# Performance work log

Hardware: AMD Instinct MI355X
Metric: run time of the kernel (lower is better)

Reference implementation:

```python
import jax, jax.numpy as jnp
import numpy as np
import math

# Dims chosen per input_specs
B, Q, S, T = 8, 64, 64, 64          # batch, queries, stat (segment) count, tokens per segment
H, DH = 8, 64                        # heads, head dim
NH = H * DH                          # num_hiddens = 512
STAT_K, TOKEN_K = 8, 16
NEG = -1e6


def setup_inputs() -> dict:
    key = jax.random.key(0)
    ks = jax.random.split(key, 11)
    f = lambda k, sh: jax.random.normal(k, sh, dtype=jnp.float32)
    w = lambda k: f(k, (NH, NH)) * 0.05  # Linear weights stored as [in, out]
    return {
        "queries": f(ks[0], (B, Q, NH)),
        "stat_keys": f(ks[1], (B, S, NH)),
        "token_keys": f(ks[2], (B * S, T, NH)),
        "values": f(ks[3], (B * S, T, NH)),
        "stat_valid_lens": jax.random.randint(ks[4], (B,), 1, S + 1, dtype=jnp.int32),
        "Wq_stat": w(ks[5]),
        "Wq_token": w(ks[6]),
        "Wk_stat": w(ks[7]),
        "Wk_token": w(ks[8]),
        "Wv": w(ks[9]),
        "Wo": w(ks[10]),
    }


def reference(queries, stat_keys, token_keys, values, stat_valid_lens,
              Wq_stat, Wq_token, Wk_stat, Wk_token, Wv, Wo):
    scale = 1.0 / math.sqrt(DH)

    def split_heads(x):  # [b, L, H*DH] -> [b, H, L, DH]
        b, L, _ = x.shape
        return x.reshape(b, L, H, DH).transpose(0, 2, 1, 3)

    q_stat = split_heads(queries @ Wq_stat)        # [B,H,Q,DH]
    q_tok = split_heads(queries @ Wq_token)        # [B,H,Q,DH]
    k_stat = split_heads(stat_keys @ Wk_stat)      # [B,H,S,DH]
    # token_keys/values come in as [B*S, T, size]; per-head layout [B,H,S,T,DH]
    k_tok = (token_keys @ Wk_token).reshape(B, S, T, H, DH).transpose(0, 3, 1, 2, 4)
    v = (values @ Wv).reshape(B, S, T, H, DH).transpose(0, 3, 1, 2, 4)

    # --- stat-level scores, valid-length mask, top-k sparsification, softmax ---
    stat_scores = jnp.einsum('bhqd,bhsd->bhqs', q_stat, k_stat) * scale  # [B,H,Q,S]
    valid = jnp.arange(S)[None, None, None, :] < stat_valid_lens[:, None, None, None]
    stat_scores = jnp.where(valid, stat_scores, NEG)
    k1 = min(S - 1, STAT_K)
    _, top_idx = jax.lax.top_k(stat_scores, k1)                           # [B,H,Q,k1]
    keep = jax.nn.one_hot(top_idx, S, dtype=stat_scores.dtype).sum(-2) > 0  # [B,H,Q,S]
    stat_w = jax.nn.softmax(jnp.where(keep, stat_scores, NEG), axis=-1)   # [B,H,Q,S]

    # --- token-level scores. NOTE: the original code computes torch.topk but then
    # overwrites with the LAST k2 positions (token_weights[:, :, -k2:] = ...), so the
    # token top-k result is dead code; we faithfully reproduce the last-k2 masking. ---
    tok_scores = jnp.einsum('bhqd,bhstd->bhsqt', q_tok, k_tok) * scale    # [B,H,S,Q,T]
    k2 = min(T - 1, TOKEN_K)
    last_mask = jnp.arange(T) >= (T - k2)
    tok_w = jax.nn.softmax(jnp.where(last_mask, tok_scores, NEG), axis=-1)
    tok_w = tok_w.transpose(0, 1, 3, 2, 4)                                # [B,H,Q,S,T]

    # --- combine hierarchy and attend over values ---
    comb = stat_w[..., None] * tok_w                                      # [B,H,Q,S,T]
    out = jnp.einsum('bhqst,bhstd->bhqd', comb, v)                        # [B,H,Q,DH]
    out = out.transpose(0, 2, 1, 3).reshape(B, Q, NH)
    return out @ Wo
```

## Files before the change

kernel.cpp:

```cpp
#include <hip/hip_runtime.h>
#include <hip/hip_bf16.h>

#define BB 8
#define QQ 64
#define SS 64
#define TT 64
#define HH 8
#define DH 64
#define NHID 512
#define STAT_K 8
#define TOKEN_K 16

typedef short bf16x8 __attribute__((ext_vector_type(8)));
typedef float f32x4 __attribute__((ext_vector_type(4)));

__device__ inline ushort f2bf_rne(float x) {
    union { float f; unsigned u; } v; v.f = x;
    unsigned r = v.u + 0x7fff + ((v.u >> 16) & 1);
    return (ushort)(r >> 16);
}
__device__ inline float bf2f(ushort h) {
    union { unsigned u; float f; } v; v.u = ((unsigned)h) << 16;
    return v.f;
}

__global__ __launch_bounds__(256) void conv_all(
    const float* w0, const float* w1, const float* w2,
    const float* w3, const float* w4, const float* w5,
    const float* queries, const float* stat_keys,
    ushort* wT, ushort* q_hi, ushort* q_lo, ushort* sk_hi, ushort* sk_lo)
{
    const int z = blockIdx.z;
    if (z < 6) {
        const float* srcs[6] = {w0, w1, w2, w3, w4, w5};
        const float* src = srcs[z];
        ushort* hi = wT + (size_t)z * 524288;
        ushort* lo = hi + 262144;
        __shared__ float t[32][33];
        const int c0 = blockIdx.x * 32, r0 = blockIdx.y * 32;
        const int tx = threadIdx.x & 31, ty = threadIdx.x >> 5;
        #pragma unroll
        for (int i = 0; i < 4; ++i)
            t[ty + 8 * i][tx] = src[(r0 + ty + 8 * i) * 512 + c0 + tx];
        __syncthreads();
        #pragma unroll
        for (int i = 0; i < 4; ++i) {
            float x = t[tx][ty + 8 * i];
            ushort h = f2bf_rne(x);
            int o = (c0 + ty + 8 * i) * 512 + r0 + tx;
            hi[o] = h;
            lo[o] = f2bf_rne(x - bf2f(h));
        }
    } else {
        const float* src = (z == 6) ? queries : stat_keys;
        ushort* hi = (z == 6) ? q_hi : sk_hi;
        ushort* lo = (z == 6) ? q_lo : sk_lo;
        int base = (blockIdx.y * 16 + blockIdx.x) * 1024 + threadIdx.x * 4;
        float4 x = *(const float4*)(src + base);
        ushort4 h, l;
        h.x = f2bf_rne(x.x); l.x = f2bf_rne(x.x - bf2f(h.x));
        h.y = f2bf_rne(x.y); l.y = f2bf_rne(x.y - bf2f(h.y));
        h.z = f2bf_rne(x.z); l.z = f2bf_rne(x.z - bf2f(h.z));
        h.w = f2bf_rne(x.w); l.w = f2bf_rne(x.w - bf2f(h.w));
        *(ushort4*)(hi + base) = h;
        *(ushort4*)(lo + base) = l;
    }
}

__global__ __launch_bounds__(256) void gemm_split3(
    const ushort* __restrict__ q_hi, const ushort* __restrict__ q_lo,
    const ushort* __restrict__ sk_hi, const ushort* __restrict__ sk_lo,
    const ushort* __restrict__ wT,
    float* __restrict__ q_stat, float* __restrict__ k_stat,
    float* __restrict__ q_tokf)
{
    const int z = blockIdx.z;
    const ushort* Ah = (z == 1) ? sk_hi : q_hi;
    const ushort* Al = (z == 1) ? sk_lo : q_lo;
    const ushort* Bh = wT + (size_t)z * 524288;
    const ushort* Bl = Bh + 262144;
    float* C = (z == 0) ? q_stat : (z == 1) ? k_stat : q_tokf;
    const int K = 512, N = 512;

    __shared__ ushort As[2][64][40];
    __shared__ ushort Bs[2][64][40];
    const int tid = threadIdx.x;
    const int row0 = blockIdx.y * 64, col0 = blockIdx.x * 64;
    const int wave = tid >> 6, lane = tid & 63;
    const int wm = wave & 1, wn = wave >> 1;
    const int m16 = lane & 15, quad = lane >> 4;
    const int srow = tid >> 2, schunk = tid & 3;

    f32x4 acc[2][2];
    #pragma unroll
    for (int i = 0; i < 2; ++i)
        #pragma unroll
        for (int j = 0; j < 2; ++j)
            #pragma unroll
            for (int r = 0; r < 4; ++r) acc[i][j][r] = 0.f;

    for (int k0 = 0; k0 < K; k0 += 32) {
        const size_t aoff = (size_t)(row0 + srow) * K + k0 + schunk * 8;
        const size_t boff = (size_t)(col0 + srow) * K + k0 + schunk * 8;
        *(uint4*)&As[0][srow][schunk * 8] = *(const uint4*)(Ah + aoff);
        *(uint4*)&Bs[0][srow][schunk * 8] = *(const uint4*)(Bh + boff);
        *(uint4*)&As[1][srow][schunk * 8] = *(const uint4*)(Al + aoff);
        *(uint4*)&Bs[1][srow][schunk * 8] = *(const uint4*)(Bl + boff);
        __syncthreads();

        bf16x8 af[2], bf[2], afl[2], bfl[2];
        #pragma unroll
        for (int i = 0; i < 2; ++i) {
            af[i]  = *(const bf16x8*)&As[0][wm * 32 + i * 16 + m16][quad * 8];
            bf[i]  = *(const bf16x8*)&Bs[0][wn * 32 + i * 16 + m16][quad * 8];
            afl[i] = *(const bf16x8*)&As[1][wm * 32 + i * 16 + m16][quad * 8];
            bfl[i] = *(const bf16x8*)&Bs[1][wn * 32 + i * 16 + m16][quad * 8];
        }
        #pragma unroll
        for (int i = 0; i < 2; ++i)
            #pragma unroll
            for (int j = 0; j < 2; ++j) {
                acc[i][j] = __builtin_amdgcn_mfma_f32_16x16x32_bf16(af[i], bf[j], acc[i][j], 0, 0, 0);
                acc[i][j] = __builtin_amdgcn_mfma_f32_16x16x32_bf16(af[i], bfl[j], acc[i][j], 0, 0, 0);
                acc[i][j] = __builtin_amdgcn_mfma_f32_16x16x32_bf16(afl[i], bf[j], acc[i][j], 0, 0, 0);
            }
        __syncthreads();
    }

    #pragma unroll
    for (int i = 0; i < 2; ++i)
        #pragma unroll
        for (int j = 0; j < 2; ++j) {
            int r0 = row0 + wm * 32 + i * 16 + quad * 4;
            int c = col0 + wn * 32 + j * 16 + m16;
            #pragma unroll
            for (int reg = 0; reg < 4; ++reg)
                C[(size_t)(r0 + reg) * N + c] = acc[i][j][reg];
        }
}

__global__ __launch_bounds__(256) void gemm_out(
    const ushort* __restrict__ Ah, const ushort* __restrict__ Al,
    const ushort* __restrict__ Bh, const ushort* __restrict__ Bl,
    float* __restrict__ C)
{
    const int K = 512, N = 512;
    __shared__ ushort As[2][64][40];
    __shared__ ushort Bs[2][64][40];
    const int tid = threadIdx.x;
    const int row0 = blockIdx.y * 64, col0 = blockIdx.x * 64;
    const int wave = tid >> 6, lane = tid & 63;
    const int wm = wave & 1, wn = wave >> 1;
    const int m16 = lane & 15, quad = lane >> 4;
    const int srow = tid >> 2, schunk = tid & 3;

    f32x4 acc[2][2];
    #pragma unroll
    for (int i = 0; i < 2; ++i)
        #pragma unroll
        for (int j = 0; j < 2; ++j)
            #pragma unroll
            for (int r = 0; r < 4; ++r) acc[i][j][r] = 0.f;

    for (int k0 = 0; k0 < K; k0 += 32) {
        const size_t aoff = (size_t)(row0 + srow) * K + k0 + schunk * 8;
        const size_t boff = (size_t)(col0 + srow) * K + k0 + schunk * 8;
        *(uint4*)&As[0][srow][schunk * 8] = *(const uint4*)(Ah + aoff);
        *(uint4*)&Bs[0][srow][schunk * 8] = *(const uint4*)(Bh + boff);
        *(uint4*)&As[1][srow][schunk * 8] = *(const uint4*)(Al + aoff);
        *(uint4*)&Bs[1][srow][schunk * 8] = *(const uint4*)(Bl + boff);
        __syncthreads();

        bf16x8 af[2], bf[2], afl[2], bfl[2];
        #pragma unroll
        for (int i = 0; i < 2; ++i) {
            af[i]  = *(const bf16x8*)&As[0][wm * 32 + i * 16 + m16][quad * 8];
            bf[i]  = *(const bf16x8*)&Bs[0][wn * 32 + i * 16 + m16][quad * 8];
            afl[i] = *(const bf16x8*)&As[1][wm * 32 + i * 16 + m16][quad * 8];
            bfl[i] = *(const bf16x8*)&Bs[1][wn * 32 + i * 16 + m16][quad * 8];
        }
        #pragma unroll
        for (int i = 0; i < 2; ++i)
            #pragma unroll
            for (int j = 0; j < 2; ++j) {
                acc[i][j] = __builtin_amdgcn_mfma_f32_16x16x32_bf16(af[i], bf[j], acc[i][j], 0, 0, 0);
                acc[i][j] = __builtin_amdgcn_mfma_f32_16x16x32_bf16(af[i], bfl[j], acc[i][j], 0, 0, 0);
                acc[i][j] = __builtin_amdgcn_mfma_f32_16x16x32_bf16(afl[i], bf[j], acc[i][j], 0, 0, 0);
            }
        __syncthreads();
    }

    #pragma unroll
    for (int i = 0; i < 2; ++i)
        #pragma unroll
        for (int j = 0; j < 2; ++j) {
            int r0 = row0 + wm * 32 + i * 16 + quad * 4;
            int c = col0 + wn * 32 + j * 16 + m16;
            #pragma unroll
            for (int reg = 0; reg < 4; ++reg)
                C[(size_t)(r0 + reg) * N + c] = acc[i][j][reg];
        }
}

__global__ __launch_bounds__(256) void gemm_tok(
    const float* __restrict__ token_keys, const float* __restrict__ values,
    const ushort* __restrict__ wkt_h, const ushort* __restrict__ wv_h,
    ushort* __restrict__ k_tok, ushort* __restrict__ v_projT)
{
    const int z = blockIdx.z;
    const float* A = z ? values : token_keys;
    const ushort* Bh = z ? wv_h : wkt_h;
    const int K = 512, N = 512;

    __shared__ ushort As[64][40];
    __shared__ ushort Bs[256][40];
    const int tid = threadIdx.x;
    const int row0 = blockIdx.y * 64, col0 = blockIdx.x * 256;
    const int wave = tid >> 6, lane = tid & 63;
    const int m16 = lane & 15, quad = lane >> 4;
    const int srow = tid >> 2, schunk = tid & 3;

    const int r = row0 + srow;
    const size_t arow = (size_t)((r >> 4) * 64 + 48 + (r & 15)) * K;

    f32x4 acc[4][4];
    #pragma unroll
    for (int i = 0; i < 4; ++i)
        #pragma unroll
        for (int j = 0; j < 4; ++j)
            #pragma unroll
            for (int rr = 0; rr < 4; ++rr) acc[i][j][rr] = 0.f;

    for (int k0 = 0; k0 < K; k0 += 32) {
        const float* ap = A + arow + k0 + schunk * 8;
        float4 x0 = ((const float4*)ap)[0];
        float4 x1 = ((const float4*)ap)[1];
        ushort4 h0, h1;
        h0.x = f2bf_rne(x0.x); h0.y = f2bf_rne(x0.y);
        h0.z = f2bf_rne(x0.z); h0.w = f2bf_rne(x0.w);
        h1.x = f2bf_rne(x1.x); h1.y = f2bf_rne(x1.y);
        h1.z = f2bf_rne(x1.z); h1.w = f2bf_rne(x1.w);
        *(ushort4*)&As[srow][schunk * 8] = h0;
        *(ushort4*)&As[srow][schunk * 8 + 4] = h1;
        #pragma unroll
        for (int i = 0; i < 4; ++i) {
            int v = tid + i * 256;
            int brow = v >> 2, bchunk = v & 3;
            *(uint4*)&Bs[brow][bchunk * 8] =
                *(const uint4*)(Bh + (size_t)(col0 + brow) * K + k0 + bchunk * 8);
        }
        __syncthreads();

        bf16x8 af[4], bf[4];
        #pragma unroll
        for (int i = 0; i < 4; ++i) {
            af[i] = *(const bf16x8*)&As[i * 16 + m16][quad * 8];
            bf[i] = *(const bf16x8*)&Bs[wave * 64 + i * 16 + m16][quad * 8];
        }
        #pragma unroll
        for (int i = 0; i < 4; ++i)
            #pragma unroll
            for (int j = 0; j < 4; ++j)
                acc[i][j] = __builtin_amdgcn_mfma_f32_16x16x32_bf16(af[i], bf[j], acc[i][j], 0, 0, 0);
        __syncthreads();
    }

    #pragma unroll
    for (int i = 0; i < 4; ++i)
        #pragma unroll
        for (int j = 0; j < 4; ++j) {
            int rg = row0 + i * 16 + quad * 4;
            int c = col0 + wave * 64 + j * 16 + m16;
            if (z == 0) {
                #pragma unroll
                for (int reg = 0; reg < 4; ++reg)
                    k_tok[(size_t)(rg + reg) * N + c] = f2bf_rne(acc[i][j][reg]);
            } else {
                int bb = rg >> 10, st = rg & 1023;
                int hh = c >> 6, dd = c & 63;
                ushort4 o4;
                o4.x = f2bf_rne(acc[i][j][0]);
                o4.y = f2bf_rne(acc[i][j][1]);
                o4.z = f2bf_rne(acc[i][j][2]);
                o4.w = f2bf_rne(acc[i][j][3]);
                *(ushort4*)(v_projT + (((size_t)((bb * 8 + hh) * 64 + dd)) << 10) + st) = o4;
            }
        }
}

__global__ __launch_bounds__(64) void stat_topk(
    const float* __restrict__ q_stat, const float* __restrict__ k_stat,
    const int* __restrict__ valid_lens,
    float* __restrict__ stat_wd)
{
    const int bid = blockIdx.x;
    const int b = bid >> 9;
    const int hq = bid & 511;
    const int h = hq >> 6;
    const int q = hq & 63;
    const int lane = threadIdx.x;

    __shared__ float sq[64];
    sq[lane] = q_stat[(b * QQ + q) * NHID + h * DH + lane];
    __syncthreads();

    const float4* kr = (const float4*)(k_stat + (b * SS + lane) * NHID + h * DH);
    const float4* sq4 = (const float4*)sq;
    float sc = 0.f;
    #pragma unroll
    for (int i = 0; i < 16; ++i) {
        float4 a = sq4[i], kk = kr[i];
        sc += a.x * kk.x + a.y * kk.y + a.z * kk.z + a.w * kk.w;
    }
    sc *= 0.125f;
    if (lane >= valid_lens[b]) sc = -1e6f;

    const float sc_keep = sc;
    float my = sc;
    bool picked = false;
    float m0 = 0.f, den = 0.f;
    #pragma unroll
    for (int j = 0; j < STAT_K; ++j) {
        float v = my;
        int idx = lane;
        #pragma unroll
        for (int off = 32; off > 0; off >>= 1) {
            float ov = __shfl_down(v, off);
            int   oi = __shfl_down(idx, off);
            if (ov > v || (ov == v && oi < idx)) { v = ov; idx = oi; }
        }
        v = __shfl(v, 0);
        idx = __shfl(idx, 0);
        if (j == 0) m0 = v;
        den += __expf(v - m0);
        if (lane == idx) { my = -3e38f; picked = true; }
    }
    float w_out = picked ? __expf(sc_keep - m0) / den : 0.f;
    stat_wd[(size_t)bid * 64 + lane] = w_out;
}

__global__ __launch_bounds__(256) void tok_attend_dense(
    const float* __restrict__ q_tokf, const ushort* __restrict__ k_tok,
    const ushort* __restrict__ v_projT, const float* __restrict__ stat_wd,
    ushort* __restrict__ ctx_hi, ushort* __restrict__ ctx_lo)
{
    const int bid = blockIdx.x;
    const int bh = bid >> 2, qb = bid & 3;
    const int b = bh >> 3, h = bh & 7;
    const int tid = threadIdx.x, wave = tid >> 6, lane = tid & 63;
    const int l15 = lane & 15, g = lane >> 4;
    const int q0 = qb * 16;

    __shared__ ushort qs_hi[16][72], qs_lo[16][72];
    __shared__ float  sw[16][65];
    __shared__ ushort comb_hi[16][264], comb_lo[16][264];

    {
        const int qq = tid >> 4, c = (tid & 15) * 4;
        float4 x = *(const float4*)(q_tokf + (size_t)(b * 64 + q0 + qq) * 512 + h * 64 + c);
        ushort4 hx, lx;
        hx.x = f2bf_rne(x.x); lx.x = f2bf_rne(x.x - bf2f(hx.x));
        hx.y = f2bf_rne(x.y); lx.y = f2bf_rne(x.y - bf2f(hx.y));
        hx.z = f2bf_rne(x.z); lx.z = f2bf_rne(x.z - bf2f(hx.z));
        hx.w = f2bf_rne(x.w); lx.w = f2bf_rne(x.w - bf2f(hx.w));
        *(ushort4*)&qs_hi[qq][c] = hx;
        *(ushort4*)&qs_lo[qq][c] = lx;
        float4 y = *(const float4*)(stat_wd + (size_t)bh * 4096 + (q0 + qq) * 64 + c);
        sw[qq][c] = y.x; sw[qq][c + 1] = y.y; sw[qq][c + 2] = y.z; sw[qq][c + 3] = y.w;
    }
    __syncthreads();

    f32x4 accd;
    #pragma unroll
    for (int rr = 0; rr < 4; ++rr) accd[rr] = 0.f;

    const int swz = (l15 & 7) << 4;

    for (int ch = 0; ch < 4; ++ch) {
        const int sbase = ch * 16 + wave * 4;
        f32x4 sc[4];
        #pragma unroll
        for (int mt = 0; mt < 4; ++mt)
            #pragma unroll
            for (int rr = 0; rr < 4; ++rr) sc[mt][rr] = 0.f;

        #pragma unroll
        for (int ks = 0; ks < 2; ++ks) {
            bf16x8 bhf = *(const bf16x8*)&qs_hi[l15][ks * 32 + g * 8];
            bf16x8 blf = *(const bf16x8*)&qs_lo[l15][ks * 32 + g * 8];
            #pragma unroll
            for (int mt = 0; mt < 4; ++mt) {
                const ushort* kp = k_tok +
                    (size_t)(b * 1024 + (sbase + mt) * 16 + l15) * 512 + h * 64 + ks * 32 + g * 8;
                bf16x8 a = *(const bf16x8*)kp;
                sc[mt] = __builtin_amdgcn_mfma_f32_16x16x32_bf16(a, bhf, sc[mt], 0, 0, 0);
                sc[mt] = __builtin_amdgcn_mfma_f32_16x16x32_bf16(a, blf, sc[mt], 0, 0, 0);
            }
        }

        #pragma unroll
        for (int mt = 0; mt < 4; ++mt) {
            float e0 = __expf(sc[mt][0] * 0.125f);
            float e1 = __expf(sc[mt][1] * 0.125f);
            float e2 = __expf(sc[mt][2] * 0.125f);
            float e3 = __expf(sc[mt][3] * 0.125f);
            float den = e0 + e1 + e2 + e3;
            den += __shfl_xor(den, 16);
            den += __shfl_xor(den, 32);
            float scl = sw[l15][sbase + mt] / den;
            ushort4 hx, lx;
            float c0 = e0 * scl; hx.x = f2bf_rne(c0); lx.x = f2bf_rne(c0 - bf2f(hx.x));
            float c1 = e1 * scl; hx.y = f2bf_rne(c1); lx.y = f2bf_rne(c1 - bf2f(hx.y));
            float c2 = e2 * scl; hx.z = f2bf_rne(c2); lx.z = f2bf_rne(c2 - bf2f(hx.z));
            float c3 = e3 * scl; hx.w = f2bf_rne(c3); lx.w = f2bf_rne(c3 - bf2f(hx.w));
            int colb = (((wave * 4 + mt) * 16 + g * 4) * 2) ^ swz;
            *(ushort4*)((char*)&comb_hi[l15][0] + colb) = hx;
            *(ushort4*)((char*)&comb_lo[l15][0] + colb) = lx;
        }
        __syncthreads();

        #pragma unroll
        for (int ks = 0; ks < 8; ++ks) {
            const ushort* vp = v_projT +
                ((size_t)(bh * 64 + wave * 16 + l15) << 10) + ch * 256 + ks * 32 + g * 8;
            bf16x8 a = *(const bf16x8*)vp;
            int colb = ((ks * 32 + g * 8) * 2) ^ swz;
            bf16x8 bhf = *(const bf16x8*)((const char*)&comb_hi[l15][0] + colb);
            bf16x8 blf = *(const bf16x8*)((const char*)&comb_lo[l15][0] + colb);
            accd = __builtin_amdgcn_mfma_f32_16x16x32_bf16(a, bhf, accd, 0, 0, 0);
            accd = __builtin_amdgcn_mfma_f32_16x16x32_bf16(a, blf, accd, 0, 0, 0);
        }
        __syncthreads();
    }

    {
        size_t o = (size_t)(b * 64 + q0 + l15) * 512 + h * 64 + wave * 16 + g * 4;
        ushort4 hx, lx;
        #pragma unroll
        for (int rr = 0; rr < 4; ++rr) {
            ushort hh2 = f2bf_rne(accd[rr]);
            ((ushort*)&hx)[rr] = hh2;
            ((ushort*)&lx)[rr] = f2bf_rne(accd[rr] - bf2f(hh2));
        }
        *(ushort4*)(ctx_hi + o) = hx;
        *(ushort4*)(ctx_lo + o) = lx;
    }
}

extern "C" void kernel_launch(void* const* d_in, const int* in_sizes, int n_in,
                              void* d_out, int out_size, void* d_ws, size_t ws_size,
                              hipStream_t stream) {
    const float* queries    = (const float*)d_in[0];
    const float* stat_keys  = (const float*)d_in[1];
    const float* token_keys = (const float*)d_in[2];
    const float* values     = (const float*)d_in[3];
    const int*   valid_lens = (const int*)d_in[4];
    const float* Wq_stat    = (const float*)d_in[5];
    const float* Wq_token   = (const float*)d_in[6];
    const float* Wk_stat    = (const float*)d_in[7];
    const float* Wk_token   = (const float*)d_in[8];
    const float* Wv         = (const float*)d_in[9];
    const float* Wo         = (const float*)d_in[10];

    char* w = (char*)d_ws;
    ushort* wT      = (ushort*)(w + 0);
    ushort* q_hi    = (ushort*)(w + 6291456);
    ushort* q_lo    = q_hi + 262144;
    ushort* sk_hi   = (ushort*)(w + 7340032);
    ushort* sk_lo   = sk_hi + 262144;
    float*  q_stat  = (float*)(w + 8388608);
    float*  k_stat  = (float*)(w + 9437184);
    float*  q_tokf  = (float*)(w + 10485760);
    ushort* k_tok   = (ushort*)(w + 11534336);
    ushort* v_projT = (ushort*)(w + 19922944);
    ushort* ctx_hi  = (ushort*)(w + 28311552);
    ushort* ctx_lo  = ctx_hi + 262144;
    float*  stat_wd = (float*)(w + 29360128);

    ushort* wkt_h = wT + 3 * 524288;
    ushort* wv_h  = wT + 4 * 524288;
    ushort* wo_h  = wT + 5 * 524288, *wo_l = wo_h + 262144;

    conv_all<<<dim3(16, 16, 8), 256, 0, stream>>>(
        Wq_stat, Wk_stat, Wq_token, Wk_token, Wv, Wo,
        queries, stat_keys, wT, q_hi, q_lo, sk_hi, sk_lo);

    gemm_split3<<<dim3(8, 8, 3), 256, 0, stream>>>(
        q_hi, q_lo, sk_hi, sk_lo, wT, q_stat, k_stat, q_tokf);

    stat_topk<<<4096, 64, 0, stream>>>(q_stat, k_stat, valid_lens, stat_wd);

    gemm_tok<<<dim3(2, 128, 2), 256, 0, stream>>>(
        token_keys, values, wkt_h, wv_h, k_tok, v_projT);

    tok_attend_dense<<<256, 256, 0, stream>>>(
        q_tokf, k_tok, v_projT, stat_wd, ctx_hi, ctx_lo);

    gemm_out<<<dim3(8, 8), 256, 0, stream>>>(
        ctx_hi, ctx_lo, wo_h, wo_l, (float*)d_out);
}
```

Before: 230.3 us.

## Fuse weight conversion into GEMMs and merge stat top-k into attention kernel

Drops the separate weight/input bf16 split-conversion kernel: each GEMM now loads fp32 weights and activations directly and converts them to hi/lo bf16 while staging tiles in shared memory. The three small projections and the two token projections run in one launch over a flat block index. Stat scoring, top-k and softmax move inside the attention kernel. This cuts the launch count from six to three and removes intermediate round trips through global memory, at the cost of repeated per-tile conversion work and strided, transposed weight loads.

Result: slower. 252.3 us (+9.5%).

```diff
diff --git a/kernel.cpp b/kernel.cpp
--- a/kernel.cpp
+++ b/kernel.cpp
@@ -1,13 +1,6 @@
 #include <hip/hip_runtime.h>
 #include <hip/hip_bf16.h>
 
-#define BB 8
-#define QQ 64
-#define SS 64
-#define TT 64
-#define HH 8
-#define DH 64
-#define NHID 512
 #define STAT_K 8
 #define TOKEN_K 16
 
@@ -24,324 +17,199 @@
     return v.f;
 }
 
-__global__ __launch_bounds__(256) void conv_all(
-    const float* w0, const float* w1, const float* w2,
-    const float* w3, const float* w4, const float* w5,
-    const float* queries, const float* stat_keys,
-    ushort* wT, ushort* q_hi, ushort* q_lo, ushort* sk_hi, ushort* sk_lo)
-{
-    const int z = blockIdx.z;
-    if (z < 6) {
-        const float* srcs[6] = {w0, w1, w2, w3, w4, w5};
-        const float* src = srcs[z];
-        ushort* hi = wT + (size_t)z * 524288;
-        ushort* lo = hi + 262144;
-        __shared__ float t[32][33];
-        const int c0 = blockIdx.x * 32, r0 = blockIdx.y * 32;
-        const int tx = threadIdx.x & 31, ty = threadIdx.x >> 5;
-        #pragma unroll
-        for (int i = 0; i < 4; ++i)
-            t[ty + 8 * i][tx] = src[(r0 + ty + 8 * i) * 512 + c0 + tx];
-        __syncthreads();
-        #pragma unroll
-        for (int i = 0; i < 4; ++i) {
-            float x = t[tx][ty + 8 * i];
-            ushort h = f2bf_rne(x);
-            int o = (c0 + ty + 8 * i) * 512 + r0 + tx;
-            hi[o] = h;
-            lo[o] = f2bf_rne(x - bf2f(h));
-        }
-    } else {
-        const float* src = (z == 6) ? queries : stat_keys;
-        ushort* hi = (z == 6) ? q_hi : sk_hi;
-        ushort* lo = (z == 6) ? q_lo : sk_lo;
-        int base = (blockIdx.y * 16 + blockIdx.x) * 1024 + threadIdx.x * 4;
-        float4 x = *(const float4*)(src + base);
-        ushort4 h, l;
-        h.x = f2bf_rne(x.x); l.x = f2bf_rne(x.x - bf2f(h.x));
-        h.y = f2bf_rne(x.y); l.y = f2bf_rne(x.y - bf2f(h.y));
-        h.z = f2bf_rne(x.z); l.z = f2bf_rne(x.z - bf2f(h.z));
-        h.w = f2bf_rne(x.w); l.w = f2bf_rne(x.w - bf2f(h.w));
-        *(ushort4*)(hi + base) = h;
-        *(ushort4*)(lo + base) = l;
-    }
-}
-
-__global__ __launch_bounds__(256) void gemm_split3(
-    const ushort* __restrict__ q_hi, const ushort* __restrict__ q_lo,
-    const ushort* __restrict__ sk_hi, const ushort* __restrict__ sk_lo,
-    const ushort* __restrict__ wT,
+__global__ __launch_bounds__(256) void fused_gemms(
+    const float* __restrict__ queries, const float* __restrict__ stat_keys,
+    const float* __restrict__ token_keys, const float* __restrict__ values,
+    const float* __restrict__ Wq_stat, const float* __restrict__ Wk_stat,
+    const float* __restrict__ Wq_token, const float* __restrict__ Wk_token,
+    const float* __restrict__ Wv,
     float* __restrict__ q_stat, float* __restrict__ k_stat,
-    float* __restrict__ q_tokf)
-{
-    const int z = blockIdx.z;
-    const ushort* Ah = (z == 1) ? sk_hi : q_hi;
-    const ushort* Al = (z == 1) ? sk_lo : q_lo;
-    const ushort* Bh = wT + (size_t)z * 524288;
-    const ushort* Bl = Bh + 262144;
-    float* C = (z == 0) ? q_stat : (z == 1) ? k_stat : q_tokf;
-    const int K = 512, N = 512;
-
-    __shared__ ushort As[2][64][40];
-    __shared__ ushort Bs[2][64][40];
-    const int tid = threadIdx.x;
-    const int row0 = blockIdx.y * 64, col0 = blockIdx.x * 64;
-    const int wave = tid >> 6, lane = tid & 63;
-    const int wm = wave & 1, wn = wave >> 1;
-    const int m16 = lane & 15, quad = lane >> 4;
-    const int srow = tid >> 2, schunk = tid & 3;
-
-    f32x4 acc[2][2];
-    #pragma unroll
-    for (int i = 0; i < 2; ++i)
-        #pragma unroll
-        for (int j = 0; j < 2; ++j)
-            #pragma unroll
-            for (int r = 0; r < 4; ++r) acc[i][j][r] = 0.f;
-
-    for (int k0 = 0; k0 < K; k0 += 32) {
-        const size_t aoff = (size_t)(row0 + srow) * K + k0 + schunk * 8;
-        const size_t boff = (size_t)(col0 + srow) * K + k0 + schunk * 8;
-        *(uint4*)&As[0][srow][schunk * 8] = *(const uint4*)(Ah + aoff);
-        *(uint4*)&Bs[0][srow][schunk * 8] = *(const uint4*)(Bh + boff);
-        *(uint4*)&As[1][srow][schunk * 8] = *(const uint4*)(Al + aoff);
-        *(uint4*)&Bs[1][srow][schunk * 8] = *(const uint4*)(Bl + boff);
-        __syncthreads();
-
-        bf16x8 af[2], bf[2], afl[2], bfl[2];
-        #pragma unroll
-        for (int i = 0; i < 2; ++i) {
-            af[i]  = *(const bf16x8*)&As[0][wm * 32 + i * 16 + m16][quad * 8];
-            bf[i]  = *(const bf16x8*)&Bs[0][wn * 32 + i * 16 + m16][quad * 8];
-            afl[i] = *(const bf16x8*)&As[1][wm * 32 + i * 16 + m16][quad * 8];
-            bfl[i] = *(const bf16x8*)&Bs[1][wn * 32 + i * 16 + m16][quad * 8];
-        }
-        #pragma unroll
-        for (int i = 0; i < 2; ++i)
-            #pragma unroll
-            for (int j = 0; j < 2; ++j) {
-                acc[i][j] = __builtin_amdgcn_mfma_f32_16x16x32_bf16(af[i], bf[j], acc[i][j], 0, 0, 0);
-                acc[i][j] = __builtin_amdgcn_mfma_f32_16x16x32_bf16(af[i], bfl[j], acc[i][j], 0, 0, 0);
-                acc[i][j] = __builtin_amdgcn_mfma_f32_16x16x32_bf16(afl[i], bf[j], acc[i][j], 0, 0, 0);
-            }
-        __syncthreads();
-    }
-
-    #pragma unroll
-    for (int i = 0; i < 2; ++i)
-        #pragma unroll
-        for (int j = 0; j < 2; ++j) {
-            int r0 = row0 + wm * 32 + i * 16 + quad * 4;
-            int c = col0 + wn * 32 + j * 16 + m16;
-            #pragma unroll
-            for (int reg = 0; reg < 4; ++reg)
-                C[(size_t)(r0 + reg) * N + c] = acc[i][j][reg];
-        }
-}
-
-__global__ __launch_bounds__(256) void gemm_out(
-    const ushort* __restrict__ Ah, const ushort* __restrict__ Al,
-    const ushort* __restrict__ Bh, const ushort* __restrict__ Bl,
-    float* __restrict__ C)
-{
-    const int K = 512, N = 512;
-    __shared__ ushort As[2][64][40];
-    __shared__ ushort Bs[2][64][40];
-    const int tid = threadIdx.x;
-    const int row0 = blockIdx.y * 64, col0 = blockIdx.x * 64;
-    const int wave = tid >> 6, lane = tid & 63;
-    const int wm = wave & 1, wn = wave >> 1;
-    const int m16 = lane & 15, quad = lane >> 4;
-    const int srow = tid >> 2, schunk = tid & 3;
-
-    f32x4 acc[2][2];
-    #pragma unroll
-    for (int i = 0; i < 2; ++i)
-        #pragma unroll
-        for (int j = 0; j < 2; ++j)
-            #pragma unroll
-            for (int r = 0; r < 4; ++r) acc[i][j][r] = 0.f;
-
-    for (int k0 = 0; k0 < K; k0 += 32) {
-        const size_t aoff = (size_t)(row0 + srow) * K + k0 + schunk * 8;
-        const size_t boff = (size_t)(col0 + srow) * K + k0 + schunk * 8;
-        *(uint4*)&As[0][srow][schunk * 8] = *(const uint4*)(Ah + aoff);
-        *(uint4*)&Bs[0][srow][schunk * 8] = *(const uint4*)(Bh + boff);
-        *(uint4*)&As[1][srow][schunk * 8] = *(const uint4*)(Al + aoff);
-        *(uint4*)&Bs[1][srow][schunk * 8] = *(const uint4*)(Bl + boff);
-        __syncthreads();
-
-        bf16x8 af[2], bf[2], afl[2], bfl[2];
-        #pragma unroll
-        for (int i = 0; i < 2; ++i) {
-            af[i]  = *(const bf16x8*)&As[0][wm * 32 + i * 16 + m16][quad * 8];
-            bf[i]  = *(const bf16x8*)&Bs[0][wn * 32 + i * 16 + m16][quad * 8];
-            afl[i] = *(const bf16x8*)&As[1][wm * 32 + i * 16 + m16][quad * 8];
-            bfl[i] = *(const bf16x8*)&Bs[1][wn * 32 + i * 16 + m16][quad * 8];
-        }
-        #pragma unroll
-        for (int i = 0; i < 2; ++i)
-            #pragma unroll
-            for (int j = 0; j < 2; ++j) {
-                acc[i][j] = __builtin_amdgcn_mfma_f32_16x16x32_bf16(af[i], bf[j], acc[i][j], 0, 0, 0);
-                acc[i][j] = __builtin_amdgcn_mfma_f32_16x16x32_bf16(af[i], bfl[j], acc[i][j], 0, 0, 0);
-                acc[i][j] = __builtin_amdgcn_mfma_f32_16x16x32_bf16(afl[i], bf[j], acc[i][j], 0, 0, 0);
-            }
-        __syncthreads();
-    }
-
-    #pragma unroll
-    for (int i = 0; i < 2; ++i)
-        #pragma unroll
-        for (int j = 0; j < 2; ++j) {
-            int r0 = row0 + wm * 32 + i * 16 + quad * 4;
-            int c = col0 + wn * 32 + j * 16 + m16;
-            #pragma unroll
-            for (int reg = 0; reg < 4; ++reg)
-                C[(size_t)(r0 + reg) * N + c] = acc[i][j][reg];
-        }
-}
-
-__global__ __launch_bounds__(256) void gemm_tok(
-    const float* __restrict__ token_keys, const float* __restrict__ values,
-    const ushort* __restrict__ wkt_h, const ushort* __restrict__ wv_h,
+    float* __restrict__ q_tokf,
     ushort* __restrict__ k_tok, ushort* __restrict__ v_projT)
 {
-    const int z = blockIdx.z;
-    const float* A = z ? values : token_keys;
-    const ushort* Bh = z ? wv_h : wkt_h;
-    const int K = 512, N = 512;
-
-    __shared__ ushort As[64][40];
-    __shared__ ushort Bs[256][40];
+    __shared__ ushort smem[12800];
     const int tid = threadIdx.x;
-    const int row0 = blockIdx.y * 64, col0 = blockIdx.x * 256;
+    const int bid = blockIdx.x;
     const int wave = tid >> 6, lane = tid & 63;
     const int m16 = lane & 15, quad = lane >> 4;
     const int srow = tid >> 2, schunk = tid & 3;
 
-    const int r = row0 + srow;
-    const size_t arow = (size_t)((r >> 4) * 64 + 48 + (r & 15)) * K;
-
-    f32x4 acc[4][4];
-    #pragma unroll
-    for (int i = 0; i < 4; ++i)
-        #pragma unroll
-        for (int j = 0; j < 4; ++j)
-            #pragma unroll
-            for (int rr = 0; rr < 4; ++rr) acc[i][j][rr] = 0.f;
-
-    for (int k0 = 0; k0 < K; k0 += 32) {
-        const float* ap = A + arow + k0 + schunk * 8;
-        float4 x0 = ((const float4*)ap)[0];
-        float4 x1 = ((const float4*)ap)[1];
-        ushort4 h0, h1;
-        h0.x = f2bf_rne(x0.x); h0.y = f2bf_rne(x0.y);
-        h0.z = f2bf_rne(x0.z); h0.w = f2bf_rne(x0.w);
-        h1.x = f2bf_rne(x1.x); h1.y = f2bf_rne(x1.y);
-        h1.z = f2bf_rne(x1.z); h1.w = f2bf_rne(x1.w);
-        *(ushort4*)&As[srow][schunk * 8] = h0;
-        *(ushort4*)&As[srow][schunk * 8 + 4] = h1;
-        #pragma unroll
-        for (int i = 0; i < 4; ++i) {
-            int v = tid + i * 256;
-            int brow = v >> 2, bchunk = v & 3;
-            *(uint4*)&Bs[brow][bchunk * 8] =
-                *(const uint4*)(Bh + (size_t)(col0 + brow) * K + k0 + bchunk * 8);
-        }
-        __syncthreads();
-
-        bf16x8 af[4], bf[4];
-        #pragma unroll
-        for (int i = 0; i < 4; ++i) {
-            af[i] = *(const bf16x8*)&As[i * 16 + m16][quad * 8];
-            bf[i] = *(const bf16x8*)&Bs[wave * 64 + i * 16 + m16][quad * 8];
-        }
+    if (bid < 192) {
+        const int z = bid >> 6, t = bid & 63;
+        const int row0 = (t >> 3) * 64, col0 = (t & 7) * 64;
+        const float* A = (z == 1) ? stat_keys : queries;
+        const float* W = (z == 0) ? Wq_stat : (z == 1) ? Wk_stat : Wq_token;
+        float* C = (z == 0) ? q_stat : (z == 1) ? k_stat : q_tokf;
+
+        ushort* As_hi = smem;
+        ushort* As_lo = smem + 2560;
+        ushort* Bs_hi = smem + 5120;
+        ushort* Bs_lo = smem + 7680;
+        const int wm = wave & 1, wn = wave >> 1;
+        const int bn0 = (tid & 15) * 4, bk2 = (tid >> 4) * 2;
+
+        f32x4 acc[2][2];
+        #pragma unroll
+        for (int i = 0; i < 2; ++i)
+            #pragma unroll
+            for (int j = 0; j < 2; ++j)
+                #pragma unroll
+                for (int r = 0; r < 4; ++r) acc[i][j][r] = 0.f;
+
+        for (int k0 = 0; k0 < 512; k0 += 32) {
+            const float* ap = A + (size_t)(row0 + srow) * 512 + k0 + schunk * 8;
+            float4 x0 = ((const float4*)ap)[0];
+            float4 x1 = ((const float4*)ap)[1];
+            ushort4 h0, l0, h1, l1;
+            h0.x = f2bf_rne(x0.x); l0.x = f2bf_rne(x0.x - bf2f(h0.x));
+            h0.y = f2bf_rne(x0.y); l0.y = f2bf_rne(x0.y - bf2f(h0.y));
+            h0.z = f2bf_rne(x0.z); l0.z = f2bf_rne(x0.z - bf2f(h0.z));
+            h0.w = f2bf_rne(x0.w); l0.w = f2bf_rne(x0.w - bf2f(h0.w));
+            h1.x = f2bf_rne(x1.x); l1.x = f2bf_rne(x1.x - bf2f(h1.x));
+            h1.y = f2bf_rne(x1.y); l1.y = f2bf_rne(x1.y - bf2f(h1.y));
+            h1.z = f2bf_rne(x1.z); l1.z = f2bf_rne(x1.z - bf2f(h1.z));
+            h1.w = f2bf_rne(x1.w); l1.w = f2bf_rne(x1.w - bf2f(h1.w));
+            *(ushort4*)&As_hi[srow * 40 + schunk * 8]     = h0;
+            *(ushort4*)&As_hi[srow * 40 + schunk * 8 + 4] = h1;
+            *(ushort4*)&As_lo[srow * 40 + schunk * 8]     = l0;
+            *(ushort4*)&As_lo[srow * 40 + schunk * 8 + 4] = l1;
+
+            const float* wp = W + (size_t)(k0 + bk2) * 512 + col0 + bn0;
+            float4 b0 = *(const float4*)wp;
+            float4 b1 = *(const float4*)(wp + 512);
+            const float* b0p = (const float*)&b0;
+            const float* b1p = (const float*)&b1;
+            #pragma unroll
+            for (int j = 0; j < 4; ++j) {
+                float v0 = b0p[j], v1 = b1p[j];
+                ushort hh0 = f2bf_rne(v0), hh1 = f2bf_rne(v1);
+                ushort ll0 = f2bf_rne(v0 - bf2f(hh0));
+                ushort ll1 = f2bf_rne(v1 - bf2f(hh1));
+                *(uint*)&Bs_hi[(bn0 + j) * 40 + bk2] = (uint)hh0 | ((uint)hh1 << 16);
+                *(uint*)&Bs_lo[(bn0 + j) * 40 + bk2] = (uint)ll0 | ((uint)ll1 << 16);
+            }
+            __syncthreads();
+
+            bf16x8 af[2], bfv[2], afl[2], bfl[2];
+            #pragma unroll
+            for (int i = 0; i < 2; ++i) {
+                af[i]  = *(const bf16x8*)&As_hi[(wm * 32 + i * 16 + m16) * 40 + quad * 8];
+                bfv[i] = *(const bf16x8*)&Bs_hi[(wn * 32 + i * 16 + m16) * 40 + quad * 8];
+                afl[i] = *(const bf16x8*)&As_lo[(wm * 32 + i * 16 + m16) * 40 + quad * 8];
+                bfl[i] = *(const bf16x8*)&Bs_lo[(wn * 32 + i * 16 + m16) * 40 + quad * 8];
+            }
+            #pragma unroll
+            for (int i = 0; i < 2; ++i)
+                #pragma unroll
+                for (int j = 0; j < 2; ++j) {
+                    acc[i][j] = __builtin_amdgcn_mfma_f32_16x16x32_bf16(af[i],  bfv[j], acc[i][j], 0, 0, 0);
+                    acc[i][j] = __builtin_amdgcn_mfma_f32_16x16x32_bf16(af[i],  bfl[j], acc[i][j], 0, 0, 0);
+                    acc[i][j] = __builtin_amdgcn_mfma_f32_16x16x32_bf16(afl[i], bfv[j], acc[i][j], 0, 0, 0);
+                }
+            __syncthreads();
+        }
+
+        #pragma unroll
+        for (int i = 0; i < 2; ++i)
+            #pragma unroll
+            for (int j = 0; j < 2; ++j) {
+                int r0 = row0 + wm * 32 + i * 16 + quad * 4;
+                int c = col0 + wn * 32 + j * 16 + m16;
+                #pragma unroll
+                for (int reg = 0; reg < 4; ++reg)
+                    C[(size_t)(r0 + reg) * 512 + c] = acc[i][j][reg];
+            }
+    } else {
+        const int u = bid - 192;
+        const int z2 = u >> 8, vv = u & 255;
+        const int col0 = (vv & 1) * 256, row0 = (vv >> 1) * 64;
+        const float* A = z2 ? values : token_keys;
+        const float* W = z2 ? Wv : Wk_token;
+
+        ushort* As = smem;
+        ushort* Bs = smem + 2560;
+        const int r = row0 + srow;
+        const size_t arow = (size_t)((r >> 4) * 64 + 48 + (r & 15)) * 512;
+        const int n0 = (tid >> 2) * 4, kk8 = (tid & 3) * 8;
+
+        f32x4 acc[4][4];
         #pragma unroll
         for (int i = 0; i < 4; ++i)
             #pragma unroll
             for (int j = 0; j < 4; ++j)
-                acc[i][j] = __builtin_amdgcn_mfma_f32_16x16x32_bf16(af[i], bf[j], acc[i][j], 0, 0, 0);
-        __syncthreads();
-    }
-
-    #pragma unroll
-    for (int i = 0; i < 4; ++i)
-        #pragma unroll
-        for (int j = 0; j < 4; ++j) {
-            int rg = row0 + i * 16 + quad * 4;
-            int c = col0 + wave * 64 + j * 16 + m16;
-            if (z == 0) {
-                #pragma unroll
-                for (int reg = 0; reg < 4; ++reg)
-                    k_tok[(size_t)(rg + reg) * N + c] = f2bf_rne(acc[i][j][reg]);
-            } else {
-                int bb = rg >> 10, st = rg & 1023;
-                int hh = c >> 6, dd = c & 63;
-                ushort4 o4;
-                o4.x = f2bf_rne(acc[i][j][0]);
-                o4.y = f2bf_rne(acc[i][j][1]);
-                o4.z = f2bf_rne(acc[i][j][2]);
-                o4.w = f2bf_rne(acc[i][j][3]);
-                *(ushort4*)(v_projT + (((size_t)((bb * 8 + hh) * 64 + dd)) << 10) + st) = o4;
-            }
-        }
-}
-
-__global__ __launch_bounds__(64) void stat_topk(
-    const float* __restrict__ q_stat, const float* __restrict__ k_stat,
-    const int* __restrict__ valid_lens,
-    float* __restrict__ stat_wd)
-{
-    const int bid = blockIdx.x;
-    const int b = bid >> 9;
-    const int hq = bid & 511;
-    const int h = hq >> 6;
-    const int q = hq & 63;
-    const int lane = threadIdx.x;
-
-    __shared__ float sq[64];
-    sq[lane] = q_stat[(b * QQ + q) * NHID + h * DH + lane];
-    __syncthreads();
-
-    const float4* kr = (const float4*)(k_stat + (b * SS + lane) * NHID + h * DH);
-    const float4* sq4 = (const float4*)sq;
-    float sc = 0.f;
-    #pragma unroll
-    for (int i = 0; i < 16; ++i) {
-        float4 a = sq4[i], kk = kr[i];
-        sc += a.x * kk.x + a.y * kk.y + a.z * kk.z + a.w * kk.w;
-    }
-    sc *= 0.125f;
-    if (lane >= valid_lens[b]) sc = -1e6f;
-
-    const float sc_keep = sc;
-    float my = sc;
-    bool picked = false;
-    float m0 = 0.f, den = 0.f;
-    #pragma unroll
-    for (int j = 0; j < STAT_K; ++j) {
-        float v = my;
-        int idx = lane;
-        #pragma unroll
-        for (int off = 32; off > 0; off >>= 1) {
-            float ov = __shfl_down(v, off);
-            int   oi = __shfl_down(idx, off);
-            if (ov > v || (ov == v && oi < idx)) { v = ov; idx = oi; }
-        }
-        v = __shfl(v, 0);
-        idx = __shfl(idx, 0);
-        if (j == 0) m0 = v;
-        den += __expf(v - m0);
-        if (lane == idx) { my = -3e38f; picked = true; }
-    }
-    float w_out = picked ? __expf(sc_keep - m0) / den : 0.f;
-    stat_wd[(size_t)bid * 64 + lane] = w_out;
-}
-
-__global__ __launch_bounds__(256) void tok_attend_dense(
-    const float* __restrict__ q_tokf, const ushort* __restrict__ k_tok,
-    const ushort* __restrict__ v_projT, const float* __restrict__ stat_wd,
+                #pragma unroll
+                for (int rr = 0; rr < 4; ++rr) acc[i][j][rr] = 0.f;
+
+        for (int k0 = 0; k0 < 512; k0 += 32) {
+            const float* ap = A + arow + k0 + schunk * 8;
+            float4 x0 = ((const float4*)ap)[0];
+            float4 x1 = ((const float4*)ap)[1];
+            ushort4 h0, h1;
+            h0.x = f2bf_rne(x0.x); h0.y = f2bf_rne(x0.y);
+            h0.z = f2bf_rne(x0.z); h0.w = f2bf_rne(x0.w);
+            h1.x = f2bf_rne(x1.x); h1.y = f2bf_rne(x1.y);
+            h1.z = f2bf_rne(x1.z); h1.w = f2bf_rne(x1.w);
+            *(ushort4*)&As[srow * 40 + schunk * 8]     = h0;
+            *(ushort4*)&As[srow * 40 + schunk * 8 + 4] = h1;
+
+            const float* wb = W + (size_t)(k0 + kk8) * 512 + col0 + n0;
+            float4 bb[8];
+            #pragma unroll
+            for (int rr = 0; rr < 8; ++rr) bb[rr] = *(const float4*)(wb + rr * 512);
+            #pragma unroll
+            for (int j = 0; j < 4; ++j) {
+                #pragma unroll
+                for (int p = 0; p < 4; ++p) {
+                    float v0 = ((const float*)&bb[2 * p])[j];
+                    float v1 = ((const float*)&bb[2 * p + 1])[j];
+                    *(uint*)&Bs[(n0 + j) * 40 + kk8 + 2 * p] =
+                        (uint)f2bf_rne(v0) | ((uint)f2bf_rne(v1) << 16);
+                }
+            }
+            __syncthreads();
+
+            bf16x8 af[4], bf[4];
+            #pragma unroll
+            for (int i = 0; i < 4; ++i) {
+                af[i] = *(const bf16x8*)&As[(i * 16 + m16) * 40 + quad * 8];
+                bf[i] = *(const bf16x8*)&Bs[(wave * 64 + i * 16 + m16) * 40 + quad * 8];
+            }
+            #pragma unroll
+            for (int i = 0; i < 4; ++i)
+                #pragma unroll
+                for (int j = 0; j < 4; ++j)
+                    acc[i][j] = __builtin_amdgcn_mfma_f32_16x16x32_bf16(af[i], bf[j], acc[i][j], 0, 0, 0);
+            __syncthreads();
+        }
+
+        #pragma unroll
+        for (int i = 0; i < 4; ++i)
+            #pragma unroll
+            for (int j = 0; j < 4; ++j) {
+                int rg = row0 + i * 16 + quad * 4;
+                int c = col0 + wave * 64 + j * 16 + m16;
+                if (z2 == 0) {
+                    #pragma unroll
+                    for (int reg = 0; reg < 4; ++reg)
+                        k_tok[(size_t)(rg + reg) * 512 + c] = f2bf_rne(acc[i][j][reg]);
+                } else {
+                    int bb2 = rg >> 10, st = rg & 1023;
+                    int hh = c >> 6, dd = c & 63;
+                    ushort4 o4;
+                    o4.x = f2bf_rne(acc[i][j][0]);
+                    o4.y = f2bf_rne(acc[i][j][1]);
+                    o4.z = f2bf_rne(acc[i][j][2]);
+                    o4.w = f2bf_rne(acc[i][j][3]);
+                    *(ushort4*)(v_projT + (((size_t)((bb2 * 8 + hh) * 64 + dd)) << 10) + st) = o4;
+                }
+            }
+    }
+}
+
+__global__ __launch_bounds__(256) void fused_attend(
+    const float* __restrict__ q_tokf, const float* __restrict__ q_stat,
+    const float* __restrict__ k_stat, const int* __restrict__ valid_lens,
+    const ushort* __restrict__ k_tok, const ushort* __restrict__ v_projT,
     ushort* __restrict__ ctx_hi, ushort* __restrict__ ctx_lo)
 {
     const int bid = blockIdx.x;
@@ -351,6 +219,8 @@
     const int l15 = lane & 15, g = lane >> 4;
     const int q0 = qb * 16;
 
+    __shared__ float  ks[64][68];
+    __shared__ float  qsf[16][68];
     __shared__ ushort qs_hi[16][72], qs_lo[16][72];
     __shared__ float  sw[16][65];
     __shared__ ushort comb_hi[16][264], comb_lo[16][264];
@@ -365,8 +235,51 @@
         hx.w = f2bf_rne(x.w); lx.w = f2bf_rne(x.w - bf2f(hx.w));
         *(ushort4*)&qs_hi[qq][c] = hx;
         *(ushort4*)&qs_lo[qq][c] = lx;
-        float4 y = *(const float4*)(stat_wd + (size_t)bh * 4096 + (q0 + qq) * 64 + c);
-        sw[qq][c] = y.x; sw[qq][c + 1] = y.y; sw[qq][c + 2] = y.z; sw[qq][c + 3] = y.w;
+        *(float4*)&qsf[qq][c] =
+            *(const float4*)(q_stat + (size_t)(b * 64 + q0 + qq) * 512 + h * 64 + c);
+        const int s = tid >> 2, c0 = (tid & 3) * 16;
+        const float* kp = k_stat + (size_t)(b * 64 + s) * 512 + h * 64 + c0;
+        #pragma unroll
+        for (int i = 0; i < 4; ++i)
+            *(float4*)&ks[s][c0 + 4 * i] = *(const float4*)(kp + 4 * i);
+    }
+    const int valid = valid_lens[b];
+    __syncthreads();
+
+    #pragma unroll
+    for (int qi = 0; qi < 4; ++qi) {
+        const int qq = wave * 4 + qi;
+        const float4* kr = (const float4*)&ks[lane][0];
+        const float4* qr = (const float4*)&qsf[qq][0];
+        float sc = 0.f;
+        #pragma unroll
+        for (int i = 0; i < 16; ++i) {
+            float4 a = qr[i], kk = kr[i];
+            sc += a.x * kk.x + a.y * kk.y + a.z * kk.z + a.w * kk.w;
+        }
+        sc *= 0.125f;
+        if (lane >= valid) sc = -1e6f;
+        const float sc_keep = sc;
+        float my = sc;
+        bool picked = false;
+        float m0 = 0.f, den = 0.f;
+        #pragma unroll
+        for (int j = 0; j < STAT_K; ++j) {
+            float v = my;
+            int idx = lane;
+            #pragma unroll
+            for (int off = 32; off > 0; off >>= 1) {
+                float ov = __shfl_down(v, off);
+                int   oi = __shfl_down(idx, off);
+                if (ov > v || (ov == v && oi < idx)) { v = ov; idx = oi; }
+            }
+            v = __shfl(v, 0);
+            idx = __shfl(idx, 0);
+            if (j == 0) m0 = v;
+            den += __expf(v - m0);
+            if (lane == idx) { my = -3e38f; picked = true; }
+        }
+        sw[qq][lane] = picked ? __expf(sc_keep - m0) / den : 0.f;
     }
     __syncthreads();
 
@@ -385,13 +298,13 @@
             for (int rr = 0; rr < 4; ++rr) sc[mt][rr] = 0.f;
 
         #pragma unroll
-        for (int ks = 0; ks < 2; ++ks) {
-            bf16x8 bhf = *(const bf16x8*)&qs_hi[l15][ks * 32 + g * 8];
-            bf16x8 blf = *(const bf16x8*)&qs_lo[l15][ks * 32 + g * 8];
+        for (int ks2 = 0; ks2 < 2; ++ks2) {
+            bf16x8 bhf = *(const bf16x8*)&qs_hi[l15][ks2 * 32 + g * 8];
+            bf16x8 blf = *(const bf16x8*)&qs_lo[l15][ks2 * 32 + g * 8];
             #pragma unroll
             for (int mt = 0; mt < 4; ++mt) {
                 const ushort* kp = k_tok +
-                    (size_t)(b * 1024 + (sbase + mt) * 16 + l15) * 512 + h * 64 + ks * 32 + g * 8;
+                    (size_t)(b * 1024 + (sbase + mt) * 16 + l15) * 512 + h * 64 + ks2 * 32 + g * 8;
                 bf16x8 a = *(const bf16x8*)kp;
                 sc[mt] = __builtin_amdgcn_mfma_f32_16x16x32_bf16(a, bhf, sc[mt], 0, 0, 0);
                 sc[mt] = __builtin_amdgcn_mfma_f32_16x16x32_bf16(a, blf, sc[mt], 0, 0, 0);
@@ -420,11 +333,11 @@
         __syncthreads();
 
         #pragma unroll
-        for (int ks = 0; ks < 8; ++ks) {
+        for (int ks2 = 0; ks2 < 8; ++ks2) {
             const ushort* vp = v_projT +
-                ((size_t)(bh * 64 + wave * 16 + l15) << 10) + ch * 256 + ks * 32 + g * 8;
+                ((size_t)(bh * 64 + wave * 16 + l15) << 10) + ch * 256 + ks2 * 32 + g * 8;
             bf16x8 a = *(const bf16x8*)vp;
-            int colb = ((ks * 32 + g * 8) * 2) ^ swz;
+            int colb = ((ks2 * 32 + g * 8) * 2) ^ swz;
             bf16x8 bhf = *(const bf16x8*)((const char*)&comb_hi[l15][0] + colb);
             bf16x8 blf = *(const bf16x8*)((const char*)&comb_lo[l15][0] + colb);
             accd = __builtin_amdgcn_mfma_f32_16x16x32_bf16(a, bhf, accd, 0, 0, 0);
@@ -445,6 +358,83 @@
         *(ushort4*)(ctx_hi + o) = hx;
         *(ushort4*)(ctx_lo + o) = lx;
     }
+}
+
+__global__ __launch_bounds__(256) void gemm_out_f(
+    const ushort* __restrict__ Ah, const ushort* __restrict__ Al,
+    const float* __restrict__ Wo, float* __restrict__ C)
+{
+    __shared__ ushort smem[10240];
+    ushort* As_hi = smem;
+    ushort* As_lo = smem + 2560;
+    ushort* Bs_hi = smem + 5120;
+    ushort* Bs_lo = smem + 7680;
+    const int tid = threadIdx.x;
+    const int row0 = blockIdx.y * 64, col0 = blockIdx.x * 64;
+    const int wave = tid >> 6, lane = tid & 63;
+    const int wm = wave & 1, wn = wave >> 1;
+    const int m16 = lane & 15, quad = lane >> 4;
+    const int srow = tid >> 2, schunk = tid & 3;
+    const int bn0 = (tid & 15) * 4, bk2 = (tid >> 4) * 2;
+
+    f32x4 acc[2][2];
+    #pragma unroll
+    for (int i = 0; i < 2; ++i)
+        #pragma unroll
+        for (int j = 0; j < 2; ++j)
+            #pragma unroll
+            for (int r = 0; r < 4; ++r) acc[i][j][r] = 0.f;
+
+    for (int k0 = 0; k0 < 512; k0 += 32) {
+        const size_t aoff = (size_t)(row0 + srow) * 512 + k0 + schunk * 8;
+        *(uint4*)&As_hi[srow * 40 + schunk * 8] = *(const uint4*)(Ah + aoff);
+        *(uint4*)&As_lo[srow * 40 + schunk * 8] = *(const uint4*)(Al + aoff);
+
+        const float* wp = Wo + (size_t)(k0 + bk2) * 512 + col0 + bn0;
+        float4 b0 = *(const float4*)wp;
+        float4 b1 = *(const float4*)(wp + 512);
+        const float* b0p = (const float*)&b0;
+        const float* b1p = (const float*)&b1;
+        #pragma unroll
+        for (int j = 0; j < 4; ++j) {
+            float v0 = b0p[j], v1 = b1p[j];
+            ushort hh0 = f2bf_rne(v0), hh1 = f2bf_rne(v1);
+            ushort ll0 = f2bf_rne(v0 - bf2f(hh0));
+            ushort ll1 = f2bf_rne(v1 - bf2f(hh1));
+            *(uint*)&Bs_hi[(bn0 + j) * 40 + bk2] = (uint)hh0 | ((uint)hh1 << 16);
+            *(uint*)&Bs_lo[(bn0 + j) * 40 + bk2] = (uint)ll0 | ((uint)ll1 << 16);
+        }
+        __syncthreads();
+
+        bf16x8 af[2], bfv[2], afl[2], bfl[2];
+        #pragma unroll
+        for (int i = 0; i < 2; ++i) {
+            af[i]  = *(const bf16x8*)&As_hi[(wm * 32 + i * 16 + m16) * 40 + quad * 8];
+            bfv[i] = *(const bf16x8*)&Bs_hi[(wn * 32 + i * 16 + m16) * 40 + quad * 8];
+            afl[i] = *(const bf16x8*)&As_lo[(wm * 32 + i * 16 + m16) * 40 + quad * 8];
+            bfl[i] = *(const bf16x8*)&Bs_lo[(wn * 32 + i * 16 + m16) * 40 + quad * 8];
+        }
+        #pragma unroll
+        for (int i = 0; i < 2; ++i)
+            #pragma unroll
+            for (int j = 0; j < 2; ++j) {
+                acc[i][j] = __builtin_amdgcn_mfma_f32_16x16x32_bf16(af[i],  bfv[j], acc[i][j], 0, 0, 0);
+                acc[i][j] = __builtin_amdgcn_mfma_f32_16x16x32_bf16(af[i],  bfl[j], acc[i][j], 0, 0, 0);
+                acc[i][j] = __builtin_amdgcn_mfma_f32_16x16x32_bf16(afl[i], bfv[j], acc[i][j], 0, 0, 0);
+            }
+        __syncthreads();
+    }
+
+    #pragma unroll
+    for (int i = 0; i < 2; ++i)
+        #pragma unroll
+        for (int j = 0; j < 2; ++j) {
+            int r0 = row0 + wm * 32 + i * 16 + quad * 4;
+            int c = col0 + wn * 32 + j * 16 + m16;
+            #pragma unroll
+            for (int reg = 0; reg < 4; ++reg)
+                C[(size_t)(r0 + reg) * 512 + c] = acc[i][j][reg];
+        }
 }
 
 extern "C" void kernel_launch(void* const* d_in, const int* in_sizes, int n_in,
@@ -463,39 +453,21 @@
     const float* Wo         = (const float*)d_in[10];
 
     char* w = (char*)d_ws;
-    ushort* wT      = (ushort*)(w + 0);
-    ushort* q_hi    = (ushort*)(w + 6291456);
-    ushort* q_lo    = q_hi + 262144;
-    ushort* sk_hi   = (ushort*)(w + 7340032);
-    ushort* sk_lo   = sk_hi + 262144;
-    float*  q_stat  = (float*)(w + 8388608);
-    float*  k_stat  = (float*)(w + 9437184);
-    float*  q_tokf  = (float*)(w + 10485760);
-    ushort* k_tok   = (ushort*)(w + 11534336);
-    ushort* v_projT = (ushort*)(w + 19922944);
-    ushort* ctx_hi  = (ushort*)(w + 28311552);
+    float*  q_stat  = (float*)(w + 0);
+    float*  k_stat  = (float*)(w + 1048576);
+    float*  q_tokf  = (float*)(w + 2097152);
+    ushort* k_tok   = (ushort*)(w + 3145728);
+    ushort* v_projT = (ushort*)(w + 11534336);
+    ushort* ctx_hi  = (ushort*)(w + 19922944);
     ushort* ctx_lo  = ctx_hi + 262144;
-    float*  stat_wd = (float*)(w + 29360128);
-
-    ushort* wkt_h = wT + 3 * 524288;
-    ushort* wv_h  = wT + 4 * 524288;
-    ushort* wo_h  = wT + 5 * 524288, *wo_l = wo_h + 262144;
-
-    conv_all<<<dim3(16, 16, 8), 256, 0, stream>>>(
-        Wq_stat, Wk_stat, Wq_token, Wk_token, Wv, Wo,
-        queries, stat_keys, wT, q_hi, q_lo, sk_hi, sk_lo);
-
-    gemm_split3<<<dim3(8, 8, 3), 256, 0, stream>>>(
-        q_hi, q_lo, sk_hi, sk_lo, wT, q_stat, k_stat, q_tokf);
-
-    stat_topk<<<4096, 64, 0, stream>>>(q_stat, k_stat, valid_lens, stat_wd);
-
-    gemm_tok<<<dim3(2, 128, 2), 256, 0, stream>>>(
-        token_keys, values, wkt_h, wv_h, k_tok, v_projT);
-
-    tok_attend_dense<<<256, 256, 0, stream>>>(
-        q_tokf, k_tok, v_projT, stat_wd, ctx_hi, ctx_lo);
-
-    gemm_out<<<dim3(8, 8), 256, 0, stream>>>(
-        ctx_hi, ctx_lo, wo_h, wo_l, (float*)d_out);
-}
+
+    fused_gemms<<<704, 256, 0, stream>>>(
+        queries, stat_keys, token_keys, values,
+        Wq_stat, Wk_stat, Wq_token, Wk_token, Wv,
+        q_stat, k_stat, q_tokf, k_tok, v_projT);
+
+    fused_attend<<<256, 256, 0, stream>>>(
+        q_tokf, q_stat, k_stat, valid_lens, k_tok, v_projT, ctx_hi, ctx_lo);
+
+    gemm_out_f<<<dim3(8, 8), 256, 0, stream>>>(ctx_hi, ctx_lo, Wo, (float*)d_out);
+}
```
